# Optimization experiments

Hardware: AMD Instinct MI355X
Metric: run time of the kernel (lower is better)

Reference implementation:

```python
import jax, jax.numpy as jnp
import numpy as np

N = 50000       # nodes
E = 1600000     # edges (avg degree 32)
DIM = 256       # args.dim (input feature dim)
OUT = 64        # args.n_classes (output dim)
ALPHA = 0.2     # leaky relu negative slope


def setup_inputs() -> dict:
    key = jax.random.key(0)
    k1, k2, k3, k4 = jax.random.split(key, 4)
    x = jax.random.normal(k1, (N, DIM), dtype=jnp.float32)
    # sparse adjacency as COO indices: row 0 = src (output row), row 1 = dst (neighbor)
    edge_index = jax.random.randint(k2, (2, E), 0, N, dtype=jnp.int32)
    # xavier-uniform init as in SpGraphAttentionLayer
    lim_w = float(np.sqrt(6.0 / (DIM + OUT)))
    W = jax.random.uniform(k3, (DIM, OUT), minval=-lim_w, maxval=lim_w, dtype=jnp.float32)
    lim_a = float(np.sqrt(6.0 / (1 + 2 * OUT)))
    a = jax.random.uniform(k4, (2 * OUT,), minval=-lim_a, maxval=lim_a, dtype=jnp.float32)
    return {"x": x, "edge_index": edge_index, "W": W, "a": a}


def reference(x, edge_index, W, a):
    # h = x @ W : [N, OUT]
    h = x @ W
    src = edge_index[0]  # [E] output row index i
    dst = edge_index[1]  # [E] neighbor index j
    # attention logit per edge: a . concat(h[i], h[j])
    logits = h[src] @ a[:OUT] + h[dst] @ a[OUT:]          # [E]
    # edge_e = exp(-leakyrelu(logits))  (note the negation, as in SpGraphAttentionLayer)
    e = jnp.exp(-jax.nn.leaky_relu(logits, ALPHA))         # [E]
    # row-wise normalizer: sum_j e_ij
    rowsum = jax.ops.segment_sum(e, src, num_segments=N)   # [N]
    # aggregated messages: sum_j e_ij * h_j
    agg = jax.ops.segment_sum(e[:, None] * h[dst], src, num_segments=N)  # [N, OUT]
    # h' = agg / rowsum, then elu (concat=True branch)
    return jax.nn.elu(agg / rowsum[:, None])
```

## Files before the change

kernel.cpp:

```cpp
#include <hip/hip_runtime.h>

#define NN 50000
#define NE 1600000
#define DIM 256
#define OUTD 64
#define ALPHA 0.2f

#define BSH 6
#define NB ((NN + 63) >> 6)
#define CAP 3072
#define CAPH 1792
#define P1 250
#define EPB (NE / P1)

#define GB1024 ((NN + 255) / 256)
#define FAT_GRID (GB1024 + P1)
#define WSTRIDE 264

typedef unsigned short u16;
typedef unsigned int u32;
typedef __attribute__((ext_vector_type(8))) short short8;
typedef __attribute__((ext_vector_type(4))) float floatx4;

__device__ __forceinline__ u16 f2bf(float f) {
  u32 b = __float_as_uint(f);
  b += 0x7FFFu + ((b >> 16) & 1u);
  return (u16)(b >> 16);
}
__device__ __forceinline__ float bflo(u32 u) { return __uint_as_float(u << 16); }
__device__ __forceinline__ float bfhi(u32 u) { return __uint_as_float(u & 0xFFFF0000u); }

__global__ __launch_bounds__(256) void init_kernel(const float* __restrict__ W,
                                                   u32* __restrict__ wt,
                                                   int* __restrict__ bktcnt) {
  if (blockIdx.x < 4) {
    const int i = blockIdx.x * 256 + threadIdx.x;
    if (i < NB) bktcnt[i] = 0;
    return;
  }
  const int g = (blockIdx.x - 4) * 256 + threadIdx.x;
  const int n = g >> 7;
  const int kp = g & 127;
  const float lo = W[(size_t)(2 * kp) * OUTD + n];
  const float hi = W[(size_t)(2 * kp + 1) * OUTD + n];
  wt[g] = (u32)f2bf(lo) | ((u32)f2bf(hi) << 16);
}

__global__ __launch_bounds__(1024) void fat_kernel(
    const float* __restrict__ x, const u32* __restrict__ wt,
    const float* __restrict__ a, u16* __restrict__ hb,
    float* __restrict__ s1, float* __restrict__ s2,
    const int* __restrict__ src, const int* __restrict__ dst,
    int* __restrict__ bktcnt, u32* __restrict__ binned)
{
  __shared__ u16 Wl[OUTD * WSTRIDE];
  int* lh = (int*)Wl;
  const int t = threadIdx.x;

  if (blockIdx.x < GB1024) {
    {
      const uint4* srcv = (const uint4*)wt;
#pragma unroll
      for (int i = 0; i < 2; ++i) {
        const int c = t + 1024 * i;
        const int n = c >> 5;
        const int k8 = c & 31;
        *(uint4*)&Wl[n * WSTRIDE + k8 * 8] = srcv[c];
      }
    }
    __syncthreads();

    const int lane = t & 63;
    const int wv = t >> 6;
    const int n = lane & 15;
    const int quad = lane >> 4;
    int rb = blockIdx.x * 256 + wv * 16;
    if (rb > NN - 16) rb = NN - 16;
    const int row = rb + n;
    const float4* xrow = (const float4*)(x + (size_t)row * DIM);

    floatx4 acc[4] = {{0.f, 0.f, 0.f, 0.f},
                      {0.f, 0.f, 0.f, 0.f},
                      {0.f, 0.f, 0.f, 0.f},
                      {0.f, 0.f, 0.f, 0.f}};

#pragma unroll
    for (int kk = 0; kk < 8; ++kk) {
      const float4 lo = xrow[kk * 8 + quad * 2];
      const float4 hi = xrow[kk * 8 + quad * 2 + 1];
      union { u32 u[4]; short8 s; } af;
      af.u[0] = (u32)f2bf(lo.x) | ((u32)f2bf(lo.y) << 16);
      af.u[1] = (u32)f2bf(lo.z) | ((u32)f2bf(lo.w) << 16);
      af.u[2] = (u32)f2bf(hi.x) | ((u32)f2bf(hi.y) << 16);
      af.u[3] = (u32)f2bf(hi.z) | ((u32)f2bf(hi.w) << 16);
#pragma unroll
      for (int nt = 0; nt < 4; ++nt) {
        const short8 bf =
            *(const short8*)&Wl[(nt * 16 + n) * WSTRIDE + kk * 32 + quad * 8];
        acc[nt] = __builtin_amdgcn_mfma_f32_16x16x32_bf16(af.s, bf, acc[nt], 0, 0, 0);
      }
    }

    float av1[4], av2[4];
#pragma unroll
    for (int nt = 0; nt < 4; ++nt) {
      av1[nt] = a[nt * 16 + n];
      av2[nt] = a[OUTD + nt * 16 + n];
    }

#pragma unroll
    for (int reg = 0; reg < 4; ++reg) {
      const int r = rb + quad * 4 + reg;
      float q1 = acc[0][reg] * av1[0] + acc[1][reg] * av1[1] +
                 acc[2][reg] * av1[2] + acc[3][reg] * av1[3];
      float q2 = acc[0][reg] * av2[0] + acc[1][reg] * av2[1] +
                 acc[2][reg] * av2[2] + acc[3][reg] * av2[3];
#pragma unroll
      for (int off = 1; off <= 8; off <<= 1) {
        q1 += __shfl_xor(q1, off);
        q2 += __shfl_xor(q2, off);
      }
      if (n == 0) { s1[r] = q1; s2[r] = q2; }
#pragma unroll
      for (int nt = 0; nt < 4; ++nt)
        hb[(size_t)r * OUTD + nt * 16 + n] = f2bf(acc[nt][reg]);
    }
    return;
  }

  const int p = blockIdx.x - GB1024;
  for (int i = t; i < NB; i += 1024) lh[i] = 0;
  __syncthreads();

  const int4* src4 = (const int4*)(src + p * EPB);
  const int4* dst4 = (const int4*)(dst + p * EPB);
  for (int i = t; i < EPB / 4; i += 1024) {
    const int4 s = src4[i];
    if ((u32)s.x < (u32)NN) atomicAdd(&lh[s.x >> BSH], 1);
    if ((u32)s.y < (u32)NN) atomicAdd(&lh[s.y >> BSH], 1);
    if ((u32)s.z < (u32)NN) atomicAdd(&lh[s.z >> BSH], 1);
    if ((u32)s.w < (u32)NN) atomicAdd(&lh[s.w >> BSH], 1);
  }
  __syncthreads();

  for (int b = t; b < NB; b += 1024) {
    const int c = lh[b];
    lh[b] = (c > 0) ? atomicAdd(bktcnt + b, c) + b * CAP : 0;
  }
  __syncthreads();

  for (int i = t; i < EPB / 4; i += 1024) {
    const int4 s = src4[i];
    const int4 d = dst4[i];
    int pos, b;
    if ((u32)s.x < (u32)NN) {
      b = s.x >> BSH; pos = atomicAdd(&lh[b], 1);
      if (pos < (b + 1) * CAP) binned[pos] = ((u32)(s.x & 63) << 16) | (u32)(d.x & 0xFFFF);
    }
    if ((u32)s.y < (u32)NN) {
      b = s.y >> BSH; pos = atomicAdd(&lh[b], 1);
      if (pos < (b + 1) * CAP) binned[pos] = ((u32)(s.y & 63) << 16) | (u32)(d.y & 0xFFFF);
    }
    if ((u32)s.z < (u32)NN) {
      b = s.z >> BSH; pos = atomicAdd(&lh[b], 1);
      if (pos < (b + 1) * CAP) binned[pos] = ((u32)(s.z & 63) << 16) | (u32)(d.z & 0xFFFF);
    }
    if ((u32)s.w < (u32)NN) {
      b = s.w >> BSH; pos = atomicAdd(&lh[b], 1);
      if (pos < (b + 1) * CAP) binned[pos] = ((u32)(s.w & 63) << 16) | (u32)(d.w & 0xFFFF);
    }
  }
}

__global__ __launch_bounds__(256) void bucket_agg_kernel(
    const u16* __restrict__ hb, const float* __restrict__ s1,
    const float* __restrict__ s2, const int* __restrict__ bktcnt,
    const u32* __restrict__ binned, float* __restrict__ out)
{
  __shared__ u32 ebuf[CAPH];
  __shared__ u16 sdst[CAPH];
  __shared__ float wls[CAPH];
  __shared__ float s1l[32];
  __shared__ int cnt[32];
  __shared__ int off0[32];
  __shared__ int cur[32];
  __shared__ int ecur;
  const int b = blockIdx.x >> 1;
  const int sub = blockIdx.x & 1;
  const int t = threadIdx.x;
  int n = bktcnt[b];
  if (n > CAP) n = CAP;

  if (t < 32) {
    cnt[t] = 0;
    const int nd = b * 64 + sub * 32 + t;
    s1l[t] = (nd < NN) ? s1[nd] : 0.f;
  }
  if (t == 0) ecur = 0;
  __syncthreads();

  const u32* eb = binned + (size_t)b * CAP;
  for (int i = t; i < n; i += 256) {
    const u32 v = eb[i];
    const int ln = (v >> 16) & 63;
    if ((ln >> 5) == sub) {
      const int pos = atomicAdd(&ecur, 1);
      if (pos < CAPH) {
        ebuf[pos] = v;
        atomicAdd(&cnt[ln & 31], 1);
      }
    }
  }
  __syncthreads();

  int nh = ecur;
  if (nh > CAPH) nh = CAPH;

  if (t < 32) {
    const int v = cnt[t];
    int xx = v;
#pragma unroll
    for (int o = 1; o < 32; o <<= 1) {
      const int y = __shfl_up(xx, o, 32);
      if (t >= o) xx += y;
    }
    off0[t] = xx - v;
    cur[t] = xx - v;
  }
  __syncthreads();

  for (int i = t; i < nh; i += 256) {
    const u32 v = ebuf[i];
    const int ln = (v >> 16) & 31;
    const int d = (int)(v & 0xFFFFu);
    const int pos = atomicAdd(&cur[ln], 1);
    sdst[pos] = (u16)d;
    const float logit = s1l[ln] + s2[d];
    const float lr = logit > 0.f ? logit : ALPHA * logit;
    wls[pos] = __expf(-lr);
  }
  __syncthreads();

  const int lane = t & 63;
  const int wv = t >> 6;
  const int g = lane >> 3;
  const int seg = lane & 7;

  for (int ni = 0; ni < 8; ++ni) {
    const int ln = wv * 8 + ni;
    const int node = b * 64 + sub * 32 + ln;
    if (node >= NN) continue;
    const int base = off0[ln];
    const int cend = base + cnt[ln];

    float a0 = 0.f, a1 = 0.f, a2 = 0.f, a3 = 0.f;
    float a4 = 0.f, a5 = 0.f, a6 = 0.f, a7 = 0.f;
    float wsum = 0.f;

    int e = base + g;
    for (; e + 24 < cend; e += 32) {
      const int dg0 = sdst[e];       const float wg0 = wls[e];
      const int dg1 = sdst[e + 8];   const float wg1 = wls[e + 8];
      const int dg2 = sdst[e + 16];  const float wg2 = wls[e + 16];
      const int dg3 = sdst[e + 24];  const float wg3 = wls[e + 24];
      const uint4 p0 = *(const uint4*)(hb + (size_t)dg0 * OUTD + seg * 8);
      const uint4 p1 = *(const uint4*)(hb + (size_t)dg1 * OUTD + seg * 8);
      const uint4 p2 = *(const uint4*)(hb + (size_t)dg2 * OUTD + seg * 8);
      const uint4 p3 = *(const uint4*)(hb + (size_t)dg3 * OUTD + seg * 8);
      a0 = fmaf(wg0, bflo(p0.x), a0); a1 = fmaf(wg0, bfhi(p0.x), a1);
      a2 = fmaf(wg0, bflo(p0.y), a2); a3 = fmaf(wg0, bfhi(p0.y), a3);
      a4 = fmaf(wg0, bflo(p0.z), a4); a5 = fmaf(wg0, bfhi(p0.z), a5);
      a6 = fmaf(wg0, bflo(p0.w), a6); a7 = fmaf(wg0, bfhi(p0.w), a7);
      wsum += wg0;
      a0 = fmaf(wg1, bflo(p1.x), a0); a1 = fmaf(wg1, bfhi(p1.x), a1);
      a2 = fmaf(wg1, bflo(p1.y), a2); a3 = fmaf(wg1, bfhi(p1.y), a3);
      a4 = fmaf(wg1, bflo(p1.z), a4); a5 = fmaf(wg1, bfhi(p1.z), a5);
      a6 = fmaf(wg1, bflo(p1.w), a6); a7 = fmaf(wg1, bfhi(p1.w), a7);
      wsum += wg1;
      a0 = fmaf(wg2, bflo(p2.x), a0); a1 = fmaf(wg2, bfhi(p2.x), a1);
      a2 = fmaf(wg2, bflo(p2.y), a2); a3 = fmaf(wg2, bfhi(p2.y), a3);
      a4 = fmaf(wg2, bflo(p2.z), a4); a5 = fmaf(wg2, bfhi(p2.z), a5);
      a6 = fmaf(wg2, bflo(p2.w), a6); a7 = fmaf(wg2, bfhi(p2.w), a7);
      wsum += wg2;
      a0 = fmaf(wg3, bflo(p3.x), a0); a1 = fmaf(wg3, bfhi(p3.x), a1);
      a2 = fmaf(wg3, bflo(p3.y), a2); a3 = fmaf(wg3, bfhi(p3.y), a3);
      a4 = fmaf(wg3, bflo(p3.z), a4); a5 = fmaf(wg3, bfhi(p3.z), a5);
      a6 = fmaf(wg3, bflo(p3.w), a6); a7 = fmaf(wg3, bfhi(p3.w), a7);
      wsum += wg3;
    }
    for (; e < cend; e += 8) {
      const int dg = sdst[e];
      const float wg = wls[e];
      const uint4 p = *(const uint4*)(hb + (size_t)dg * OUTD + seg * 8);
      a0 = fmaf(wg, bflo(p.x), a0);
      a1 = fmaf(wg, bfhi(p.x), a1);
      a2 = fmaf(wg, bflo(p.y), a2);
      a3 = fmaf(wg, bfhi(p.y), a3);
      a4 = fmaf(wg, bflo(p.z), a4);
      a5 = fmaf(wg, bfhi(p.z), a5);
      a6 = fmaf(wg, bflo(p.w), a6);
      a7 = fmaf(wg, bfhi(p.w), a7);
      wsum += wg;
    }

#pragma unroll
    for (int off = 8; off <= 32; off <<= 1) {
      a0 += __shfl_xor(a0, off);
      a1 += __shfl_xor(a1, off);
      a2 += __shfl_xor(a2, off);
      a3 += __shfl_xor(a3, off);
      a4 += __shfl_xor(a4, off);
      a5 += __shfl_xor(a5, off);
      a6 += __shfl_xor(a6, off);
      a7 += __shfl_xor(a7, off);
      wsum += __shfl_xor(wsum, off);
    }

    if (g == 0) {
      const float inv = (cnt[ln] > 0) ? 1.f / wsum : 0.f;
      float4 r;
      float v;
      v = a0 * inv; r.x = v > 0.f ? v : (__expf(v) - 1.f);
      v = a1 * inv; r.y = v > 0.f ? v : (__expf(v) - 1.f);
      v = a2 * inv; r.z = v > 0.f ? v : (__expf(v) - 1.f);
      v = a3 * inv; r.w = v > 0.f ? v : (__expf(v) - 1.f);
      *(float4*)(out + (size_t)node * OUTD + seg * 8) = r;
      v = a4 * inv; r.x = v > 0.f ? v : (__expf(v) - 1.f);
      v = a5 * inv; r.y = v > 0.f ? v : (__expf(v) - 1.f);
      v = a6 * inv; r.z = v > 0.f ? v : (__expf(v) - 1.f);
      v = a7 * inv; r.w = v > 0.f ? v : (__expf(v) - 1.f);
      *(float4*)(out + (size_t)node * OUTD + seg * 8 + 4) = r;
    }
  }
}

extern "C" void kernel_launch(void* const* d_in, const int* in_sizes, int n_in,
                              void* d_out, int out_size, void* d_ws, size_t ws_size,
                              hipStream_t stream) {
  const float* x = (const float*)d_in[0];
  const int* ei = (const int*)d_in[1];
  const float* W = (const float*)d_in[2];
  const float* a = (const float*)d_in[3];
  float* out = (float*)d_out;

  u16* hb = (u16*)d_ws;
  float* s1 = (float*)(hb + (size_t)NN * OUTD);
  float* s2 = s1 + NN;
  int* bktcnt = (int*)(s2 + NN);
  u32* wt = (u32*)(bktcnt + NB);
  u32* binned = wt + 8192;

  const int* src = ei;
  const int* dst = ei + NE;

  hipLaunchKernelGGL(init_kernel, dim3(36), dim3(256), 0, stream, W, wt, bktcnt);
  hipLaunchKernelGGL(fat_kernel, dim3(FAT_GRID), dim3(1024), 0, stream,
                     x, wt, a, hb, s1, s2, src, dst, bktcnt, binned);
  hipLaunchKernelGGL(bucket_agg_kernel, dim3(2 * NB), dim3(256), 0, stream,
                     hb, s1, s2, bktcnt, binned, out);
}
```

Baseline: 151.7 us.

## Drop shared edge staging buffer and assign one node per 8-lane group

The aggregation kernel stops staging this half-bucket's edges in a shared ebuf with a global atomic cursor. It now counts edges per node directly from the global binned list, then rereads that list to scatter destinations and weights into CSR order. The gather loop is also reorganised so each 8-lane group owns one node and walks all of its edges alone. This removes the cross-lane shuffle reductions and the 8-iteration per-wave node loop, and it shrinks shared memory. In exchange the binned list is read twice from global memory, and per-node edge counts now vary across lanes in a wave, so some lanes can sit idle.

```diff
diff --git a/kernel.cpp b/kernel.cpp
--- a/kernel.cpp
+++ b/kernel.cpp
@@ -177,14 +177,12 @@
     const float* __restrict__ s2, const int* __restrict__ bktcnt,
     const u32* __restrict__ binned, float* __restrict__ out)
 {
-  __shared__ u32 ebuf[CAPH];
   __shared__ u16 sdst[CAPH];
   __shared__ float wls[CAPH];
   __shared__ float s1l[32];
   __shared__ int cnt[32];
   __shared__ int off0[32];
   __shared__ int cur[32];
-  __shared__ int ecur;
   const int b = blockIdx.x >> 1;
   const int sub = blockIdx.x & 1;
   const int t = threadIdx.x;
@@ -196,25 +194,14 @@
     const int nd = b * 64 + sub * 32 + t;
     s1l[t] = (nd < NN) ? s1[nd] : 0.f;
   }
-  if (t == 0) ecur = 0;
   __syncthreads();
 
   const u32* eb = binned + (size_t)b * CAP;
   for (int i = t; i < n; i += 256) {
-    const u32 v = eb[i];
-    const int ln = (v >> 16) & 63;
-    if ((ln >> 5) == sub) {
-      const int pos = atomicAdd(&ecur, 1);
-      if (pos < CAPH) {
-        ebuf[pos] = v;
-        atomicAdd(&cnt[ln & 31], 1);
-      }
-    }
-  }
-  __syncthreads();
-
-  int nh = ecur;
-  if (nh > CAPH) nh = CAPH;
+    const int ln6 = (eb[i] >> 16) & 63;
+    if ((ln6 >> 5) == sub) atomicAdd(&cnt[ln6 & 31], 1);
+  }
+  __syncthreads();
 
   if (t < 32) {
     const int v = cnt[t];
@@ -229,15 +216,20 @@
   }
   __syncthreads();
 
-  for (int i = t; i < nh; i += 256) {
-    const u32 v = ebuf[i];
-    const int ln = (v >> 16) & 31;
-    const int d = (int)(v & 0xFFFFu);
-    const int pos = atomicAdd(&cur[ln], 1);
-    sdst[pos] = (u16)d;
-    const float logit = s1l[ln] + s2[d];
-    const float lr = logit > 0.f ? logit : ALPHA * logit;
-    wls[pos] = __expf(-lr);
+  for (int i = t; i < n; i += 256) {
+    const u32 v = eb[i];
+    const int ln6 = (v >> 16) & 63;
+    if ((ln6 >> 5) == sub) {
+      const int ln = ln6 & 31;
+      const int d = (int)(v & 0xFFFFu);
+      const int pos = atomicAdd(&cur[ln], 1);
+      if (pos < CAPH) {
+        sdst[pos] = (u16)d;
+        const float logit = s1l[ln] + s2[d];
+        const float lr = logit > 0.f ? logit : ALPHA * logit;
+        wls[pos] = __expf(-lr);
+      }
+    }
   }
   __syncthreads();
 
@@ -245,92 +237,77 @@
   const int wv = t >> 6;
   const int g = lane >> 3;
   const int seg = lane & 7;
-
-  for (int ni = 0; ni < 8; ++ni) {
-    const int ln = wv * 8 + ni;
-    const int node = b * 64 + sub * 32 + ln;
-    if (node >= NN) continue;
-    const int base = off0[ln];
-    const int cend = base + cnt[ln];
-
-    float a0 = 0.f, a1 = 0.f, a2 = 0.f, a3 = 0.f;
-    float a4 = 0.f, a5 = 0.f, a6 = 0.f, a7 = 0.f;
-    float wsum = 0.f;
-
-    int e = base + g;
-    for (; e + 24 < cend; e += 32) {
-      const int dg0 = sdst[e];       const float wg0 = wls[e];
-      const int dg1 = sdst[e + 8];   const float wg1 = wls[e + 8];
-      const int dg2 = sdst[e + 16];  const float wg2 = wls[e + 16];
-      const int dg3 = sdst[e + 24];  const float wg3 = wls[e + 24];
-      const uint4 p0 = *(const uint4*)(hb + (size_t)dg0 * OUTD + seg * 8);
-      const uint4 p1 = *(const uint4*)(hb + (size_t)dg1 * OUTD + seg * 8);
-      const uint4 p2 = *(const uint4*)(hb + (size_t)dg2 * OUTD + seg * 8);
-      const uint4 p3 = *(const uint4*)(hb + (size_t)dg3 * OUTD + seg * 8);
-      a0 = fmaf(wg0, bflo(p0.x), a0); a1 = fmaf(wg0, bfhi(p0.x), a1);
-      a2 = fmaf(wg0, bflo(p0.y), a2); a3 = fmaf(wg0, bfhi(p0.y), a3);
-      a4 = fmaf(wg0, bflo(p0.z), a4); a5 = fmaf(wg0, bfhi(p0.z), a5);
-      a6 = fmaf(wg0, bflo(p0.w), a6); a7 = fmaf(wg0, bfhi(p0.w), a7);
-      wsum += wg0;
-      a0 = fmaf(wg1, bflo(p1.x), a0); a1 = fmaf(wg1, bfhi(p1.x), a1);
-      a2 = fmaf(wg1, bflo(p1.y), a2); a3 = fmaf(wg1, bfhi(p1.y), a3);
-      a4 = fmaf(wg1, bflo(p1.z), a4); a5 = fmaf(wg1, bfhi(p1.z), a5);
-      a6 = fmaf(wg1, bflo(p1.w), a6); a7 = fmaf(wg1, bfhi(p1.w), a7);
-      wsum += wg1;
-      a0 = fmaf(wg2, bflo(p2.x), a0); a1 = fmaf(wg2, bfhi(p2.x), a1);
-      a2 = fmaf(wg2, bflo(p2.y), a2); a3 = fmaf(wg2, bfhi(p2.y), a3);
-      a4 = fmaf(wg2, bflo(p2.z), a4); a5 = fmaf(wg2, bfhi(p2.z), a5);
-      a6 = fmaf(wg2, bflo(p2.w), a6); a7 = fmaf(wg2, bfhi(p2.w), a7);
-      wsum += wg2;
-      a0 = fmaf(wg3, bflo(p3.x), a0); a1 = fmaf(wg3, bfhi(p3.x), a1);
-      a2 = fmaf(wg3, bflo(p3.y), a2); a3 = fmaf(wg3, bfhi(p3.y), a3);
-      a4 = fmaf(wg3, bflo(p3.z), a4); a5 = fmaf(wg3, bfhi(p3.z), a5);
-      a6 = fmaf(wg3, bflo(p3.w), a6); a7 = fmaf(wg3, bfhi(p3.w), a7);
-      wsum += wg3;
-    }
-    for (; e < cend; e += 8) {
-      const int dg = sdst[e];
-      const float wg = wls[e];
-      const uint4 p = *(const uint4*)(hb + (size_t)dg * OUTD + seg * 8);
-      a0 = fmaf(wg, bflo(p.x), a0);
-      a1 = fmaf(wg, bfhi(p.x), a1);
-      a2 = fmaf(wg, bflo(p.y), a2);
-      a3 = fmaf(wg, bfhi(p.y), a3);
-      a4 = fmaf(wg, bflo(p.z), a4);
-      a5 = fmaf(wg, bfhi(p.z), a5);
-      a6 = fmaf(wg, bflo(p.w), a6);
-      a7 = fmaf(wg, bfhi(p.w), a7);
-      wsum += wg;
-    }
-
-#pragma unroll
-    for (int off = 8; off <= 32; off <<= 1) {
-      a0 += __shfl_xor(a0, off);
-      a1 += __shfl_xor(a1, off);
-      a2 += __shfl_xor(a2, off);
-      a3 += __shfl_xor(a3, off);
-      a4 += __shfl_xor(a4, off);
-      a5 += __shfl_xor(a5, off);
-      a6 += __shfl_xor(a6, off);
-      a7 += __shfl_xor(a7, off);
-      wsum += __shfl_xor(wsum, off);
-    }
-
-    if (g == 0) {
-      const float inv = (cnt[ln] > 0) ? 1.f / wsum : 0.f;
-      float4 r;
-      float v;
-      v = a0 * inv; r.x = v > 0.f ? v : (__expf(v) - 1.f);
-      v = a1 * inv; r.y = v > 0.f ? v : (__expf(v) - 1.f);
-      v = a2 * inv; r.z = v > 0.f ? v : (__expf(v) - 1.f);
-      v = a3 * inv; r.w = v > 0.f ? v : (__expf(v) - 1.f);
-      *(float4*)(out + (size_t)node * OUTD + seg * 8) = r;
-      v = a4 * inv; r.x = v > 0.f ? v : (__expf(v) - 1.f);
-      v = a5 * inv; r.y = v > 0.f ? v : (__expf(v) - 1.f);
-      v = a6 * inv; r.z = v > 0.f ? v : (__expf(v) - 1.f);
-      v = a7 * inv; r.w = v > 0.f ? v : (__expf(v) - 1.f);
-      *(float4*)(out + (size_t)node * OUTD + seg * 8 + 4) = r;
-    }
+  const int ln = wv * 8 + g;
+  const int node = b * 64 + sub * 32 + ln;
+  const int base = off0[ln];
+  int myc = cnt[ln];
+  if (base >= CAPH) myc = 0;
+  else if (base + myc > CAPH) myc = CAPH - base;
+
+  float a0 = 0.f, a1 = 0.f, a2 = 0.f, a3 = 0.f;
+  float a4 = 0.f, a5 = 0.f, a6 = 0.f, a7 = 0.f;
+  float wsum = 0.f;
+
+  int e = 0;
+  for (; e + 3 < myc; e += 4) {
+    const int dg0 = sdst[base + e];      const float wg0 = wls[base + e];
+    const int dg1 = sdst[base + e + 1];  const float wg1 = wls[base + e + 1];
+    const int dg2 = sdst[base + e + 2];  const float wg2 = wls[base + e + 2];
+    const int dg3 = sdst[base + e + 3];  const float wg3 = wls[base + e + 3];
+    const uint4 p0 = *(const uint4*)(hb + (size_t)dg0 * OUTD + seg * 8);
+    const uint4 p1 = *(const uint4*)(hb + (size_t)dg1 * OUTD + seg * 8);
+    const uint4 p2 = *(const uint4*)(hb + (size_t)dg2 * OUTD + seg * 8);
+    const uint4 p3 = *(const uint4*)(hb + (size_t)dg3 * OUTD + seg * 8);
+    a0 = fmaf(wg0, bflo(p0.x), a0); a1 = fmaf(wg0, bfhi(p0.x), a1);
+    a2 = fmaf(wg0, bflo(p0.y), a2); a3 = fmaf(wg0, bfhi(p0.y), a3);
+    a4 = fmaf(wg0, bflo(p0.z), a4); a5 = fmaf(wg0, bfhi(p0.z), a5);
+    a6 = fmaf(wg0, bflo(p0.w), a6); a7 = fmaf(wg0, bfhi(p0.w), a7);
+    wsum += wg0;
+    a0 = fmaf(wg1, bflo(p1.x), a0); a1 = fmaf(wg1, bfhi(p1.x), a1);
+    a2 = fmaf(wg1, bflo(p1.y), a2); a3 = fmaf(wg1, bfhi(p1.y), a3);
+    a4 = fmaf(wg1, bflo(p1.z), a4); a5 = fmaf(wg1, bfhi(p1.z), a5);
+    a6 = fmaf(wg1, bflo(p1.w), a6); a7 = fmaf(wg1, bfhi(p1.w), a7);
+    wsum += wg1;
+    a0 = fmaf(wg2, bflo(p2.x), a0); a1 = fmaf(wg2, bfhi(p2.x), a1);
+    a2 = fmaf(wg2, bflo(p2.y), a2); a3 = fmaf(wg2, bfhi(p2.y), a3);
+    a4 = fmaf(wg2, bflo(p2.z), a4); a5 = fmaf(wg2, bfhi(p2.z), a5);
+    a6 = fmaf(wg2, bflo(p2.w), a6); a7 = fmaf(wg2, bfhi(p2.w), a7);
+    wsum += wg2;
+    a0 = fmaf(wg3, bflo(p3.x), a0); a1 = fmaf(wg3, bfhi(p3.x), a1);
+    a2 = fmaf(wg3, bflo(p3.y), a2); a3 = fmaf(wg3, bfhi(p3.y), a3);
+    a4 = fmaf(wg3, bflo(p3.z), a4); a5 = fmaf(wg3, bfhi(p3.z), a5);
+    a6 = fmaf(wg3, bflo(p3.w), a6); a7 = fmaf(wg3, bfhi(p3.w), a7);
+    wsum += wg3;
+  }
+  for (; e < myc; ++e) {
+    const int dg = sdst[base + e];
+    const float wg = wls[base + e];
+    const uint4 p = *(const uint4*)(hb + (size_t)dg * OUTD + seg * 8);
+    a0 = fmaf(wg, bflo(p.x), a0);
+    a1 = fmaf(wg, bfhi(p.x), a1);
+    a2 = fmaf(wg, bflo(p.y), a2);
+    a3 = fmaf(wg, bfhi(p.y), a3);
+    a4 = fmaf(wg, bflo(p.z), a4);
+    a5 = fmaf(wg, bfhi(p.z), a5);
+    a6 = fmaf(wg, bflo(p.w), a6);
+    a7 = fmaf(wg, bfhi(p.w), a7);
+    wsum += wg;
+  }
+
+  if (node < NN) {
+    const float inv = (myc > 0) ? 1.f / wsum : 0.f;
+    float4 r;
+    float v;
+    v = a0 * inv; r.x = v > 0.f ? v : (__expf(v) - 1.f);
+    v = a1 * inv; r.y = v > 0.f ? v : (__expf(v) - 1.f);
+    v = a2 * inv; r.z = v > 0.f ? v : (__expf(v) - 1.f);
+    v = a3 * inv; r.w = v > 0.f ? v : (__expf(v) - 1.f);
+    *(float4*)(out + (size_t)node * OUTD + seg * 8) = r;
+    v = a4 * inv; r.x = v > 0.f ? v : (__expf(v) - 1.f);
+    v = a5 * inv; r.y = v > 0.f ? v : (__expf(v) - 1.f);
+    v = a6 * inv; r.z = v > 0.f ? v : (__expf(v) - 1.f);
+    v = a7 * inv; r.w = v > 0.f ? v : (__expf(v) - 1.f);
+    *(float4*)(out + (size_t)node * OUTD + seg * 8 + 4) = r;
   }
 }
 
```

Result: faster. 142.9 us (-5.8%).
